# Kernel tuning notes

Measured on AMD Instinct MI355X. Metric: run time of the kernel, lower is better.

Reference implementation:

```python
import jax, jax.numpy as jnp
import numpy as np

B, N, D = 8, 192, 768   # batch of docs, events per doc, embed_dim
H = 150                 # Score hidden_dim
PAD = -1000.0           # pad_and_stack fill value


def setup_inputs() -> dict:
    key = jax.random.key(0)
    ks = jax.random.split(key, 7)
    s1 = 1.0 / np.sqrt(3 * D)
    s2 = 1.0 / np.sqrt(H)
    return {
        "event_embed": jax.random.normal(ks[0], (B, N, D), jnp.float32),
        "W1": jax.random.normal(ks[1], (3 * D, H), jnp.float32) * s1,
        "b1": jnp.zeros((H,), jnp.float32),
        "W2": jax.random.normal(ks[2], (H, H), jnp.float32) * s2,
        "b2": jnp.zeros((H,), jnp.float32),
        "W3": jax.random.normal(ks[3], (H, 1), jnp.float32) * s2,
        "b3": jnp.zeros((1,), jnp.float32),
    }


def reference(event_embed, W1, b1, W2, b2, W3, b3):
    Bq, Nq, Dq = event_embed.shape
    # antecedent pairs: for each event i, all k < i (row-major, matches torch loop order)
    rows, cols = jnp.tril_indices(Nq, k=-1)          # [P], P = N*(N-1)/2
    i_g = event_embed[:, rows]                        # [B, P, D]
    j_g = event_embed[:, cols]                        # [B, P, D]
    pairs = jnp.concatenate([i_g, j_g, i_g * j_g], axis=-1)  # [B, P, 3D]
    # Score MLP (dropout is identity at inference)
    h = jax.nn.relu(pairs @ W1 + b1)                  # [B, P, H]
    h = jax.nn.relu(h @ W2 + b2)                      # [B, P, H]
    s = (h @ W3 + b3)[..., 0]                         # [B, P]
    # Scatter pair scores into [B, N, N]; diagonal stays 0 = epsilon score.
    logits = jnp.zeros((Bq, Nq, Nq), event_embed.dtype).at[:, rows, cols].set(s)
    tri = jnp.tril(jnp.ones((Nq, Nq), dtype=bool))    # valid cols: k <= i (incl epsilon)
    masked = jnp.where(tri, logits, -jnp.inf)
    probs = jax.nn.softmax(masked, axis=-1)           # ragged softmax per event row
    return jnp.where(tri, probs, jnp.asarray(PAD, probs.dtype))  # pad_and_stack(value=-1000)
```

## Files before the change

kernel.cpp:

```cpp
#include <hip/hip_runtime.h>
#include <hip/hip_bf16.h>

#define NSEQ   192
#define PADV   -1000.0f
#define NEGINF -1.0e30f

typedef _Float16 f16x8 __attribute__((ext_vector_type(8)));
typedef float    f32x4 __attribute__((ext_vector_type(4)));

__device__ __forceinline__ void glds16(const void* g, void* l) {
  __builtin_amdgcn_global_load_lds(
      (const __attribute__((address_space(1))) unsigned int*)g,
      (__attribute__((address_space(3))) unsigned int*)l, 16, 0, 0);
}

#define MFMA16(a, b, c) __builtin_amdgcn_mfma_f32_16x16x32_f16((a), (b), (c), 0, 0, 0)

__global__ __launch_bounds__(256) void prep_pack(const float* __restrict__ W1,
                                                 const float* __restrict__ W2,
                                                 const float* __restrict__ b1,
                                                 _Float16* __restrict__ W1abp,
                                                 _Float16* __restrict__ W1cp,
                                                 _Float16* __restrict__ W2p,
                                                 float* __restrict__ b1p,
                                                 float* __restrict__ A12) {
  int idx = blockIdx.x * 256 + threadIdx.x;
  if (idx < 245760) { A12[idx] = 0.f; A12[245760 + idx] = 0.f; }

  if (idx < 245760) {
    int e = idx & 7, l = (idx >> 3) & 63, t = idx >> 9;
    int ct = t % 20, kk = t / 20;
    int k = kk * 32 + ((l >> 4) << 3) + e;
    int hp = ct * 16 + (l & 15);
    int col = (hp < 160) ? hp : hp - 160;
    int rbase = (hp < 160) ? 0 : 768;
    float v = (col < 150) ? W1[(size_t)(rbase + k) * 150 + col] : 0.f;
    W1abp[idx] = (_Float16)v;
  } else if (idx < 393216) {
    int j = idx - 245760;
    int kk = j / 6144, rem = j % 6144;
    int q = rem >> 9, l = (rem >> 3) & 63, e = rem & 7;
    int k = kk * 32 + ((l >> 4) << 3) + e;
    int h = q * 16 + (l & 15);
    float v = (q < 10 && h < 150) ? W1[(size_t)(1536 + k) * 150 + h] : 0.f;
    W1cp[j] = (_Float16)v;
  } else if (idx < 423936) {
    int j = idx - 393216;
    int s = j / 6144, rem = j % 6144;
    int q = rem >> 9, l = (rem >> 3) & 63, e = rem & 7;
    int k = s * 32 + ((l >> 4) << 3) + e;
    int h = q * 16 + (l & 15);
    float v = (q < 10 && k < 150 && h < 150) ? W2[(size_t)k * 150 + h] : 0.f;
    W2p[j] = (_Float16)v;
  } else if (idx < 424096) {
    int h = idx - 423936;
    b1p[h] = (h < 150) ? b1[h] : 0.f;
  }
}

__global__ __launch_bounds__(256) void prep_gemm(const float* __restrict__ E,
                                                 const _Float16* __restrict__ W1abp,
                                                 float* __restrict__ A12) {
  int tid = threadIdx.x;
  int w = tid >> 6, l = tid & 63, m = l & 15, kg = l >> 4;
  int mt = blockIdx.x >> 3;
  int c  = blockIdx.x & 7;
  const float* ep = E + (size_t)(mt * 16 + m) * 768 + c * 96;

  f32x4 acc[5];
#pragma unroll
  for (int u = 0; u < 5; ++u) acc[u] = (f32x4){0.f, 0.f, 0.f, 0.f};

#pragma unroll
  for (int kk = 0; kk < 3; ++kk) {
    int k = kk * 32 + kg * 8;
    f32x4 x0 = *(const f32x4*)(ep + k);
    f32x4 x1 = *(const f32x4*)(ep + k + 4);
    f16x8 af;
#pragma unroll
    for (int e = 0; e < 4; ++e) { af[e] = (_Float16)x0[e]; af[e + 4] = (_Float16)x1[e]; }
    const f16x8* wp = (const f16x8*)W1abp + (size_t)(((c * 3 + kk) * 20) + w * 5) * 64 + l;
#pragma unroll
    for (int u = 0; u < 5; ++u)
      acc[u] = MFMA16(af, wp[u * 64], acc[u]);
  }
#pragma unroll
  for (int u = 0; u < 5; ++u)
#pragma unroll
    for (int r = 0; r < 4; ++r)
      atomicAdd(&A12[(size_t)(mt * 16 + kg * 4 + r) * 320 + (w * 5 + u) * 16 + m], acc[u][r]);
}

__global__ __launch_bounds__(256) void pair_mlp(
    const float* __restrict__ E, const float* __restrict__ A12,
    const _Float16* __restrict__ W1cp, const _Float16* __restrict__ W2p,
    const float* __restrict__ b1p, const float* __restrict__ b2,
    const float* __restrict__ W3, const float* __restrict__ b3,
    float* __restrict__ out) {
  __shared__ alignas(16) char pool[75008];
  char* eib = pool + 24576;
  char* ejb = pool + 49152;

  const int tid = threadIdx.x;
  const int w = tid >> 6, l = tid & 63;
  const int m = l & 15, kg = l >> 4;

  int bid = blockIdx.x;
  int blk = (bid & 7) * 78 + (bid >> 3);
  int b = blk / 78, r0 = blk - b * 78;
  int it = (int)((sqrtf(8.f * (float)r0 + 1.f) - 1.f) * 0.5f);
  while (it * (it + 1) / 2 > r0) --it;
  while ((it + 1) * (it + 2) / 2 <= r0) ++it;
  int jt = r0 - it * (it + 1) / 2;

  const int ibase = b * NSEQ + it * 16;
  const int jbase = b * NSEQ + jt * 16;

#pragma unroll
  for (int q = 0; q < 3; ++q)
    glds16(W1cp + (size_t)(w * 3 + q) * 512 + l * 8, pool + (w * 3 + q) * 1024);

#pragma unroll
  for (int q = 0; q < 12; ++q) {
    int t = tid + 256 * q;
    int isI = (t < 1536);
    int tt = isI ? t : t - 1536;
    int r = tt / 96, d = tt - (tt / 96) * 96;
    int sc = d ^ (r & 7);
    const float* src = E + (size_t)((isI ? ibase : jbase) + r) * 768 + sc * 8;
    f32x4 a0 = *(const f32x4*)(src);
    f32x4 a1 = *(const f32x4*)(src + 4);
    f16x8 v;
#pragma unroll
    for (int e = 0; e < 4; ++e) { v[e] = (_Float16)a0[e]; v[e + 4] = (_Float16)a1[e]; }
    *(f16x8*)((isI ? eib : ejb) + r * 1536 + d * 16) = v;
  }

  if (tid < 160) {
    float* bwf = (float*)(pool + 73728);
    bwf[tid]       = (tid < 150) ? b2[tid] : 0.f;
    bwf[160 + tid] = (tid < 150) ? W3[tid] : 0.f;
  }
  float b3v = b3[0];

  f32x4 acc1[10][4];
#pragma unroll
  for (int ct = 0; ct < 10; ++ct) {
    f32x4 a1v = *(const f32x4*)(A12 + (size_t)(ibase + m) * 320 + ct * 16 + kg * 4);
    f32x4 b1v = *(const f32x4*)(b1p + ct * 16 + kg * 4);
#pragma unroll
    for (int pt = 0; pt < 4; ++pt) {
      f32x4 a2v = *(const f32x4*)(A12 + (size_t)(jbase + w * 4 + pt) * 320 + 160 + ct * 16 + kg * 4);
      acc1[ct][pt] = a1v + a2v + b1v;
    }
  }

  __syncthreads();

  for (int t = 0; t < 24; ++t) {
    if (t < 23) {
#pragma unroll
      for (int q = 0; q < 3; ++q)
        glds16(W1cp + ((size_t)(t + 1) * 12 + w * 3 + q) * 512 + l * 8,
               pool + ((t + 1) & 1) * 12288 + (w * 3 + q) * 1024);
      asm volatile("s_waitcnt vmcnt(3)" ::: "memory");
    } else {
      asm volatile("s_waitcnt vmcnt(0)" ::: "memory");
    }
    __builtin_amdgcn_s_barrier();

    const char* wb = pool + (t & 1) * 12288;
    int cb = t * 4 + kg;
    f16x8 eiv = *(const f16x8*)(eib + m * 1536 + ((cb ^ (m & 7)) << 4));
    f16x8 pf[4];
#pragma unroll
    for (int pt = 0; pt < 4; ++pt) {
      int jr = w * 4 + pt;
      f16x8 ejv = *(const f16x8*)(ejb + jr * 1536 + ((cb ^ (jr & 7)) << 4));
      pf[pt] = eiv * ejv;
    }
#pragma unroll
    for (int ct = 0; ct < 10; ++ct) {
      f16x8 wf = *(const f16x8*)(wb + ct * 1024 + l * 16);
#pragma unroll
      for (int pt = 0; pt < 4; ++pt)
        acc1[ct][pt] = MFMA16(wf, pf[pt], acc1[ct][pt]);
    }
    __builtin_amdgcn_s_barrier();
  }

  auto write_h1 = [&](int c, int pt) {
    char* hbp = eib + (w * 2 + c) * 6144;
#pragma unroll
    for (int ct = 0; ct < 10; ++ct) {
      union { _Float16 h[4]; unsigned u[2]; } cv;
      cv.h[0] = (_Float16)fmaxf(acc1[ct][pt][0], 0.f);
      cv.h[1] = (_Float16)fmaxf(acc1[ct][pt][1], 0.f);
      cv.h[2] = (_Float16)fmaxf(acc1[ct][pt][2], 0.f);
      cv.h[3] = (_Float16)fmaxf(acc1[ct][pt][3], 0.f);
      int cc = (2 * ct + (kg >> 1)) ^ (m & 7);
      char* dst = hbp + m * 384 + cc * 16 + (kg & 1) * 8;
      *(unsigned*)(dst)     = cv.u[0];
      *(unsigned*)(dst + 4) = cv.u[1];
    }
  };

#pragma unroll
  for (int q = 0; q < 3; ++q)
    glds16(W2p + (size_t)(w * 3 + q) * 512 + l * 8, pool + (w * 3 + q) * 1024);
  write_h1(0, 0);
  write_h1(1, 1);

  f32x4 acc2[10][2];
  float sums[2][2];

#pragma unroll
  for (int r = 0; r < 10; ++r) {
    const int p = r / 5, s = r - p * 5;
    if (r < 9) {
      int ns = (r + 1 >= 5) ? r + 1 - 5 : r + 1;
#pragma unroll
      for (int q = 0; q < 3; ++q)
        glds16(W2p + ((size_t)ns * 12 + w * 3 + q) * 512 + l * 8,
               pool + ((r + 1) & 1) * 12288 + (w * 3 + q) * 1024);
      asm volatile("s_waitcnt vmcnt(3)" ::: "memory");
    } else {
      asm volatile("s_waitcnt vmcnt(0)" ::: "memory");
    }
    __builtin_amdgcn_s_barrier();

    if (r == 5) { write_h1(0, 2); write_h1(1, 3); }
    if (s == 0) {
#pragma unroll
      for (int ct = 0; ct < 10; ++ct) {
        acc2[ct][0] = (f32x4){0.f, 0.f, 0.f, 0.f};
        acc2[ct][1] = (f32x4){0.f, 0.f, 0.f, 0.f};
      }
    }

    const char* wb = pool + (r & 1) * 12288;
    f16x8 hf[2];
#pragma unroll
    for (int c = 0; c < 2; ++c)
      hf[c] = *(const f16x8*)(eib + (w * 2 + c) * 6144 + m * 384 +
                              (((4 * s + kg) ^ (m & 7)) << 4));
#pragma unroll
    for (int ct = 0; ct < 10; ++ct) {
      f16x8 wf = *(const f16x8*)(wb + ct * 1024 + l * 16);
      acc2[ct][0] = MFMA16(wf, hf[0], acc2[ct][0]);
      acc2[ct][1] = MFMA16(wf, hf[1], acc2[ct][1]);
    }

    if (s == 4) {
      const float* bwp = (const float*)(pool + 73728);
#pragma unroll
      for (int c = 0; c < 2; ++c) {
        float sum = 0.f;
#pragma unroll
        for (int ct = 0; ct < 10; ++ct) {
          f32x4 b2q = *(const f32x4*)(bwp + ct * 16 + kg * 4);
          f32x4 w3q = *(const f32x4*)(bwp + 160 + ct * 16 + kg * 4);
#pragma unroll
          for (int r2 = 0; r2 < 4; ++r2)
            sum += fmaxf(acc2[ct][c][r2] + b2q[r2], 0.f) * w3q[r2];
        }
        sum += __shfl_xor(sum, 16, 64);
        sum += __shfl_xor(sum, 32, 64);
        sums[p][c] = sum;
      }
    }
    __builtin_amdgcn_s_barrier();
  }

  if (kg == 0) {
    int il = it * 16 + m;
#pragma unroll
    for (int p = 0; p < 2; ++p)
#pragma unroll
      for (int c = 0; c < 2; ++c) {
        int jl = jt * 16 + w * 4 + p * 2 + c;
        if (jl < il)
          out[(size_t)(b * NSEQ + il) * NSEQ + jl] = sums[p][c] + b3v;
      }
  }
}

__global__ __launch_bounds__(256) void softmax_rows(float* __restrict__ out) {
  int w = threadIdx.x >> 6, l = threadIdx.x & 63;
  int blk = blockIdx.x * 4 + w;
  int i = blk % NSEQ;
  size_t base = (size_t)blk * NSEQ;
  float v[3];
  float mx = NEGINF;
#pragma unroll
  for (int t = 0; t < 3; ++t) {
    int j = l + 64 * t;
    float x = (j < i) ? out[base + j] : (j == i ? 0.f : NEGINF);
    v[t] = x;
    mx = fmaxf(mx, x);
  }
#pragma unroll
  for (int off = 32; off >= 1; off >>= 1) mx = fmaxf(mx, __shfl_xor(mx, off, 64));
  float s = 0.f;
#pragma unroll
  for (int t = 0; t < 3; ++t) s += __expf(v[t] - mx);
#pragma unroll
  for (int off = 32; off >= 1; off >>= 1) s += __shfl_xor(s, off, 64);
  float inv = 1.0f / s;
#pragma unroll
  for (int t = 0; t < 3; ++t) {
    int j = l + 64 * t;
    out[base + j] = (j <= i) ? __expf(v[t] - mx) * inv : PADV;
  }
}

extern "C" void kernel_launch(void* const* d_in, const int* in_sizes, int n_in,
                              void* d_out, int out_size, void* d_ws, size_t ws_size,
                              hipStream_t stream) {
  const float* E  = (const float*)d_in[0];
  const float* W1 = (const float*)d_in[1];
  const float* b1 = (const float*)d_in[2];
  const float* W2 = (const float*)d_in[3];
  const float* b2 = (const float*)d_in[4];
  const float* W3 = (const float*)d_in[5];
  const float* b3 = (const float*)d_in[6];
  float* out = (float*)d_out;

  char* ws = (char*)d_ws;
  float*    A12   = (float*)(ws);
  _Float16* W1abp = (_Float16*)(ws + 1966080);
  _Float16* W1cp  = (_Float16*)(ws + 2457600);
  _Float16* W2p   = (_Float16*)(ws + 2752512);
  float*    b1p   = (float*)(ws + 2813952);

  prep_pack<<<1657, 256, 0, stream>>>(W1, W2, b1, W1abp, W1cp, W2p, b1p, A12);
  prep_gemm<<<768, 256, 0, stream>>>(E, W1abp, A12);
  pair_mlp<<<624, 256, 0, stream>>>(E, A12, W1cp, W2p, b1p, b2, W3, b3, out);
  softmax_rows<<<384, 256, 0, stream>>>(out);
}
```

Baseline: 104.2 us.

## Halve pair tile to 16x8, stream weights into registers instead of LDS

After: 91.71 us. 1.14x faster.

```diff
diff --git a/kernel.cpp b/kernel.cpp
--- a/kernel.cpp
+++ b/kernel.cpp
@@ -7,12 +7,6 @@
 
 typedef _Float16 f16x8 __attribute__((ext_vector_type(8)));
 typedef float    f32x4 __attribute__((ext_vector_type(4)));
-
-__device__ __forceinline__ void glds16(const void* g, void* l) {
-  __builtin_amdgcn_global_load_lds(
-      (const __attribute__((address_space(1))) unsigned int*)g,
-      (__attribute__((address_space(3))) unsigned int*)l, 16, 0, 0);
-}
 
 #define MFMA16(a, b, c) __builtin_amdgcn_mfma_f32_16x16x32_f16((a), (b), (c), 0, 0, 0)
 
@@ -36,24 +30,24 @@
     int rbase = (hp < 160) ? 0 : 768;
     float v = (col < 150) ? W1[(size_t)(rbase + k) * 150 + col] : 0.f;
     W1abp[idx] = (_Float16)v;
-  } else if (idx < 393216) {
+  } else if (idx < 368640) {
     int j = idx - 245760;
-    int kk = j / 6144, rem = j % 6144;
-    int q = rem >> 9, l = (rem >> 3) & 63, e = rem & 7;
+    int e = j & 7, l = (j >> 3) & 63, t = j >> 9;
+    int ct = t % 10, kk = t / 10;
     int k = kk * 32 + ((l >> 4) << 3) + e;
-    int h = q * 16 + (l & 15);
-    float v = (q < 10 && h < 150) ? W1[(size_t)(1536 + k) * 150 + h] : 0.f;
+    int h = ct * 16 + (l & 15);
+    float v = (h < 150) ? W1[(size_t)(1536 + k) * 150 + h] : 0.f;
     W1cp[j] = (_Float16)v;
-  } else if (idx < 423936) {
-    int j = idx - 393216;
-    int s = j / 6144, rem = j % 6144;
-    int q = rem >> 9, l = (rem >> 3) & 63, e = rem & 7;
+  } else if (idx < 394240) {
+    int j = idx - 368640;
+    int e = j & 7, l = (j >> 3) & 63, t = j >> 9;
+    int ct = t % 10, s = t / 10;
     int k = s * 32 + ((l >> 4) << 3) + e;
-    int h = q * 16 + (l & 15);
-    float v = (q < 10 && k < 150 && h < 150) ? W2[(size_t)k * 150 + h] : 0.f;
+    int h = ct * 16 + (l & 15);
+    float v = (k < 150 && h < 150) ? W2[(size_t)k * 150 + h] : 0.f;
     W2p[j] = (_Float16)v;
-  } else if (idx < 424096) {
-    int h = idx - 423936;
+  } else if (idx < 394400) {
+    int h = idx - 394240;
     b1p[h] = (h < 150) ? b1[h] : 0.f;
   }
 }
@@ -97,31 +91,28 @@
     const float* __restrict__ b1p, const float* __restrict__ b2,
     const float* __restrict__ W3, const float* __restrict__ b3,
     float* __restrict__ out) {
-  __shared__ alignas(16) char pool[75008];
-  char* eib = pool + 24576;
-  char* ejb = pool + 49152;
+  __shared__ alignas(16) char pool[50432];
+  char* eib = pool;
+  char* ejb = pool + 24576;
 
   const int tid = threadIdx.x;
   const int w = tid >> 6, l = tid & 63;
   const int m = l & 15, kg = l >> 4;
+  const int jr0 = 2 * w, jr1 = 2 * w + 1;
 
   int bid = blockIdx.x;
-  int blk = (bid & 7) * 78 + (bid >> 3);
-  int b = blk / 78, r0 = blk - b * 78;
-  int it = (int)((sqrtf(8.f * (float)r0 + 1.f) - 1.f) * 0.5f);
-  while (it * (it + 1) / 2 > r0) --it;
-  while ((it + 1) * (it + 2) / 2 <= r0) ++it;
-  int jt = r0 - it * (it + 1) / 2;
+  int blk = (bid & 7) * 156 + (bid >> 3);
+  int b = blk / 156, r0 = blk - b * 156;
+  int it = (int)((sqrtf(4.f * (float)r0 + 1.f) - 1.f) * 0.5f);
+  while (it * it + it > r0) --it;
+  while ((it + 1) * (it + 1) + (it + 1) <= r0) ++it;
+  int jt = r0 - it * it - it;
 
   const int ibase = b * NSEQ + it * 16;
-  const int jbase = b * NSEQ + jt * 16;
-
-#pragma unroll
-  for (int q = 0; q < 3; ++q)
-    glds16(W1cp + (size_t)(w * 3 + q) * 512 + l * 8, pool + (w * 3 + q) * 1024);
-
-#pragma unroll
-  for (int q = 0; q < 12; ++q) {
+  const int jbase = b * NSEQ + jt * 8;
+
+#pragma unroll
+  for (int q = 0; q < 9; ++q) {
     int t = tid + 256 * q;
     int isI = (t < 1536);
     int tt = isI ? t : t - 1536;
@@ -137,151 +128,127 @@
   }
 
   if (tid < 160) {
-    float* bwf = (float*)(pool + 73728);
+    float* bwf = (float*)(pool + 49152);
     bwf[tid]       = (tid < 150) ? b2[tid] : 0.f;
     bwf[160 + tid] = (tid < 150) ? W3[tid] : 0.f;
   }
   float b3v = b3[0];
 
-  f32x4 acc1[10][4];
+  f32x4 acc1[10][2];
 #pragma unroll
   for (int ct = 0; ct < 10; ++ct) {
     f32x4 a1v = *(const f32x4*)(A12 + (size_t)(ibase + m) * 320 + ct * 16 + kg * 4);
     f32x4 b1v = *(const f32x4*)(b1p + ct * 16 + kg * 4);
 #pragma unroll
-    for (int pt = 0; pt < 4; ++pt) {
-      f32x4 a2v = *(const f32x4*)(A12 + (size_t)(jbase + w * 4 + pt) * 320 + 160 + ct * 16 + kg * 4);
+    for (int pt = 0; pt < 2; ++pt) {
+      f32x4 a2v = *(const f32x4*)(A12 + (size_t)(jbase + jr0 + pt) * 320 + 160 + ct * 16 + kg * 4);
       acc1[ct][pt] = a1v + a2v + b1v;
     }
   }
 
   __syncthreads();
 
-  for (int t = 0; t < 24; ++t) {
+  f16x8 wA[10], wB[10];
+#pragma unroll
+  for (int ct = 0; ct < 10; ++ct)
+    wA[ct] = *(const f16x8*)(W1cp + (size_t)ct * 512 + l * 8);
+
+  auto step1 = [&](int t, f16x8* cur, f16x8* nxt) {
     if (t < 23) {
 #pragma unroll
-      for (int q = 0; q < 3; ++q)
-        glds16(W1cp + ((size_t)(t + 1) * 12 + w * 3 + q) * 512 + l * 8,
-               pool + ((t + 1) & 1) * 12288 + (w * 3 + q) * 1024);
-      asm volatile("s_waitcnt vmcnt(3)" ::: "memory");
-    } else {
-      asm volatile("s_waitcnt vmcnt(0)" ::: "memory");
-    }
-    __builtin_amdgcn_s_barrier();
-
-    const char* wb = pool + (t & 1) * 12288;
+      for (int ct = 0; ct < 10; ++ct)
+        nxt[ct] = *(const f16x8*)(W1cp + ((size_t)(t + 1) * 10 + ct) * 512 + l * 8);
+    }
     int cb = t * 4 + kg;
     f16x8 eiv = *(const f16x8*)(eib + m * 1536 + ((cb ^ (m & 7)) << 4));
-    f16x8 pf[4];
-#pragma unroll
-    for (int pt = 0; pt < 4; ++pt) {
-      int jr = w * 4 + pt;
-      f16x8 ejv = *(const f16x8*)(ejb + jr * 1536 + ((cb ^ (jr & 7)) << 4));
-      pf[pt] = eiv * ejv;
-    }
+    f16x8 ej0 = *(const f16x8*)(ejb + jr0 * 1536 + ((cb ^ (jr0 & 7)) << 4));
+    f16x8 ej1 = *(const f16x8*)(ejb + jr1 * 1536 + ((cb ^ (jr1 & 7)) << 4));
+    f16x8 pf0 = eiv * ej0;
+    f16x8 pf1 = eiv * ej1;
 #pragma unroll
     for (int ct = 0; ct < 10; ++ct) {
-      f16x8 wf = *(const f16x8*)(wb + ct * 1024 + l * 16);
-#pragma unroll
-      for (int pt = 0; pt < 4; ++pt)
-        acc1[ct][pt] = MFMA16(wf, pf[pt], acc1[ct][pt]);
-    }
-    __builtin_amdgcn_s_barrier();
-  }
-
-  auto write_h1 = [&](int c, int pt) {
-    char* hbp = eib + (w * 2 + c) * 6144;
+      acc1[ct][0] = MFMA16(cur[ct], pf0, acc1[ct][0]);
+      acc1[ct][1] = MFMA16(cur[ct], pf1, acc1[ct][1]);
+    }
+  };
+  for (int t = 0; t < 24; t += 2) {
+    step1(t, wA, wB);
+    step1(t + 1, wB, wA);
+  }
+
+  f16x8 vA[10], vB[10];
+#pragma unroll
+  for (int ct = 0; ct < 10; ++ct)
+    vA[ct] = *(const f16x8*)(W2p + (size_t)ct * 512 + l * 8);
+
+  asm volatile("s_waitcnt lgkmcnt(0)" ::: "memory");
+  __builtin_amdgcn_s_barrier();
+
+  auto write_h1 = [&](int c) {
+    char* hbp = pool + (w * 2 + c) * 6144;
 #pragma unroll
     for (int ct = 0; ct < 10; ++ct) {
       union { _Float16 h[4]; unsigned u[2]; } cv;
-      cv.h[0] = (_Float16)fmaxf(acc1[ct][pt][0], 0.f);
-      cv.h[1] = (_Float16)fmaxf(acc1[ct][pt][1], 0.f);
-      cv.h[2] = (_Float16)fmaxf(acc1[ct][pt][2], 0.f);
-      cv.h[3] = (_Float16)fmaxf(acc1[ct][pt][3], 0.f);
+      cv.h[0] = (_Float16)fmaxf(acc1[ct][c][0], 0.f);
+      cv.h[1] = (_Float16)fmaxf(acc1[ct][c][1], 0.f);
+      cv.h[2] = (_Float16)fmaxf(acc1[ct][c][2], 0.f);
+      cv.h[3] = (_Float16)fmaxf(acc1[ct][c][3], 0.f);
       int cc = (2 * ct + (kg >> 1)) ^ (m & 7);
       char* dst = hbp + m * 384 + cc * 16 + (kg & 1) * 8;
       *(unsigned*)(dst)     = cv.u[0];
       *(unsigned*)(dst + 4) = cv.u[1];
     }
   };
-
-#pragma unroll
-  for (int q = 0; q < 3; ++q)
-    glds16(W2p + (size_t)(w * 3 + q) * 512 + l * 8, pool + (w * 3 + q) * 1024);
-  write_h1(0, 0);
-  write_h1(1, 1);
+  write_h1(0);
+  write_h1(1);
 
   f32x4 acc2[10][2];
-  float sums[2][2];
-
-#pragma unroll
-  for (int r = 0; r < 10; ++r) {
-    const int p = r / 5, s = r - p * 5;
-    if (r < 9) {
-      int ns = (r + 1 >= 5) ? r + 1 - 5 : r + 1;
-#pragma unroll
-      for (int q = 0; q < 3; ++q)
-        glds16(W2p + ((size_t)ns * 12 + w * 3 + q) * 512 + l * 8,
-               pool + ((r + 1) & 1) * 12288 + (w * 3 + q) * 1024);
-      asm volatile("s_waitcnt vmcnt(3)" ::: "memory");
-    } else {
-      asm volatile("s_waitcnt vmcnt(0)" ::: "memory");
-    }
-    __builtin_amdgcn_s_barrier();
-
-    if (r == 5) { write_h1(0, 2); write_h1(1, 3); }
-    if (s == 0) {
-#pragma unroll
-      for (int ct = 0; ct < 10; ++ct) {
-        acc2[ct][0] = (f32x4){0.f, 0.f, 0.f, 0.f};
-        acc2[ct][1] = (f32x4){0.f, 0.f, 0.f, 0.f};
-      }
-    }
-
-    const char* wb = pool + (r & 1) * 12288;
-    f16x8 hf[2];
-#pragma unroll
-    for (int c = 0; c < 2; ++c)
-      hf[c] = *(const f16x8*)(eib + (w * 2 + c) * 6144 + m * 384 +
-                              (((4 * s + kg) ^ (m & 7)) << 4));
+#pragma unroll
+  for (int ct = 0; ct < 10; ++ct) {
+    acc2[ct][0] = (f32x4){0.f, 0.f, 0.f, 0.f};
+    acc2[ct][1] = (f32x4){0.f, 0.f, 0.f, 0.f};
+  }
+
+#pragma unroll
+  for (int s = 0; s < 5; ++s) {
+    f16x8* cur = (s & 1) ? vB : vA;
+    f16x8* nxt = (s & 1) ? vA : vB;
+    if (s < 4) {
+#pragma unroll
+      for (int ct = 0; ct < 10; ++ct)
+        nxt[ct] = *(const f16x8*)(W2p + ((size_t)(s + 1) * 10 + ct) * 512 + l * 8);
+    }
+    f16x8 hf0 = *(const f16x8*)(pool + (w * 2 + 0) * 6144 + m * 384 +
+                                (((4 * s + kg) ^ (m & 7)) << 4));
+    f16x8 hf1 = *(const f16x8*)(pool + (w * 2 + 1) * 6144 + m * 384 +
+                                (((4 * s + kg) ^ (m & 7)) << 4));
 #pragma unroll
     for (int ct = 0; ct < 10; ++ct) {
-      f16x8 wf = *(const f16x8*)(wb + ct * 1024 + l * 16);
-      acc2[ct][0] = MFMA16(wf, hf[0], acc2[ct][0]);
-      acc2[ct][1] = MFMA16(wf, hf[1], acc2[ct][1]);
-    }
-
-    if (s == 4) {
-      const float* bwp = (const float*)(pool + 73728);
-#pragma unroll
-      for (int c = 0; c < 2; ++c) {
-        float sum = 0.f;
-#pragma unroll
-        for (int ct = 0; ct < 10; ++ct) {
-          f32x4 b2q = *(const f32x4*)(bwp + ct * 16 + kg * 4);
-          f32x4 w3q = *(const f32x4*)(bwp + 160 + ct * 16 + kg * 4);
-#pragma unroll
-          for (int r2 = 0; r2 < 4; ++r2)
-            sum += fmaxf(acc2[ct][c][r2] + b2q[r2], 0.f) * w3q[r2];
-        }
-        sum += __shfl_xor(sum, 16, 64);
-        sum += __shfl_xor(sum, 32, 64);
-        sums[p][c] = sum;
-      }
-    }
-    __builtin_amdgcn_s_barrier();
-  }
-
-  if (kg == 0) {
-    int il = it * 16 + m;
-#pragma unroll
-    for (int p = 0; p < 2; ++p)
-#pragma unroll
-      for (int c = 0; c < 2; ++c) {
-        int jl = jt * 16 + w * 4 + p * 2 + c;
-        if (jl < il)
-          out[(size_t)(b * NSEQ + il) * NSEQ + jl] = sums[p][c] + b3v;
-      }
+      acc2[ct][0] = MFMA16(cur[ct], hf0, acc2[ct][0]);
+      acc2[ct][1] = MFMA16(cur[ct], hf1, acc2[ct][1]);
+    }
+  }
+
+  const float* bwp = (const float*)(pool + 49152);
+#pragma unroll
+  for (int c = 0; c < 2; ++c) {
+    float sum = 0.f;
+#pragma unroll
+    for (int ct = 0; ct < 10; ++ct) {
+      f32x4 b2q = *(const f32x4*)(bwp + ct * 16 + kg * 4);
+      f32x4 w3q = *(const f32x4*)(bwp + 160 + ct * 16 + kg * 4);
+#pragma unroll
+      for (int r2 = 0; r2 < 4; ++r2)
+        sum += fmaxf(acc2[ct][c][r2] + b2q[r2], 0.f) * w3q[r2];
+    }
+    sum += __shfl_xor(sum, 16, 64);
+    sum += __shfl_xor(sum, 32, 64);
+    if (kg == 0) {
+      int il = it * 16 + m;
+      int jl = jt * 8 + 2 * w + c;
+      if (jl < il)
+        out[(size_t)(b * NSEQ + il) * NSEQ + jl] = sum + b3v;
+    }
   }
 }
 
@@ -330,11 +297,11 @@
   float*    A12   = (float*)(ws);
   _Float16* W1abp = (_Float16*)(ws + 1966080);
   _Float16* W1cp  = (_Float16*)(ws + 2457600);
-  _Float16* W2p   = (_Float16*)(ws + 2752512);
-  float*    b1p   = (float*)(ws + 2813952);
-
-  prep_pack<<<1657, 256, 0, stream>>>(W1, W2, b1, W1abp, W1cp, W2p, b1p, A12);
+  _Float16* W2p   = (_Float16*)(ws + 2703360);
+  float*    b1p   = (float*)(ws + 2754560);
+
+  prep_pack<<<1541, 256, 0, stream>>>(W1, W2, b1, W1abp, W1cp, W2p, b1p, A12);
   prep_gemm<<<768, 256, 0, stream>>>(E, W1abp, A12);
-  pair_mlp<<<624, 256, 0, stream>>>(E, A12, W1cp, W2p, b1p, b2, W3, b3, out);
+  pair_mlp<<<1248, 256, 0, stream>>>(E, A12, W1cp, W2p, b1p, b2, W3, b3, out);
   softmax_rows<<<384, 256, 0, stream>>>(out);
 }
```
